# Kernel optimization log

Hardware: AMD Instinct MI355X
Metric: run time of the kernel (lower is better)

The kernel has to match this reference:

```python
import jax, jax.numpy as jnp
import numpy as np

T, IN, H, R = 8192, 256, 256, 4
MEM, MVD, OUT = 256, 128, 256


def lstm_scan(xs, Wih, Whh, b, reverse=False):
    # xs: [T, F]; torch LSTM gate order i, f, g, o; b = b_ih + b_hh combined
    Hh = Whh.shape[-1]

    def step(carry, x):
        h, c = carry
        z = Wih @ x + Whh @ h + b  # [4H]
        i, f, g, o = jnp.split(z, 4)
        c = jax.nn.sigmoid(f) * c + jax.nn.sigmoid(i) * jnp.tanh(g)
        h = jax.nn.sigmoid(o) * jnp.tanh(c)
        return (h, c), h

    init = (jnp.zeros((Hh,), xs.dtype), jnp.zeros((Hh,), xs.dtype))
    _, hs = jax.lax.scan(step, init, xs, reverse=reverse)
    return hs


def bilstm(xs, Wih, Whh, b):
    # Wih: [2, 4H, F] (dir 0 = forward, dir 1 = backward)
    hf = lstm_scan(xs, Wih[0], Whh[0], b[0])
    hb = lstm_scan(xs, Wih[1], Whh[1], b[1], reverse=True)
    return jnp.concatenate([hf, hb], axis=-1)


def setup_inputs() -> dict:
    key = jax.random.key(0)
    ks = jax.random.split(key, 24)
    s = 0.05
    d = {}
    d["inputs"] = jax.random.normal(ks[0], (T, IN), jnp.float32)
    d["edges"] = jax.random.randint(ks[1], (T, 2), 0, T)
    d["memory"] = jax.random.normal(ks[2], (T, MVD), jnp.float32)
    d["Wl_ih"] = jax.random.normal(ks[3], (2, 4 * H, IN)) * s
    d["Wl_hh"] = jax.random.normal(ks[4], (2, 4 * H, H)) * s
    d["bl"] = jax.random.normal(ks[5], (2, 4 * H)) * s
    d["Wh_ih"] = jax.random.normal(ks[6], (2, 4 * H, 2 * H)) * s
    d["Wh_hh"] = jax.random.normal(ks[7], (2, 4 * H, H)) * s
    d["bh"] = jax.random.normal(ks[8], (2, 4 * H)) * s
    d["Win"] = jax.random.normal(ks[9], (H, IN)) * s
    d["bin_"] = jax.random.normal(ks[10], (H,)) * s
    d["We"] = jax.random.normal(ks[11], (R, H, 2 * H)) * s
    d["be"] = jax.random.normal(ks[12], (R, H)) * s
    d["Wn_ih"] = jax.random.normal(ks[13], (R, 4 * H, IN + H)) * s
    d["Wn_hh"] = jax.random.normal(ks[14], (R, 4 * H, H)) * s
    d["bn"] = jax.random.normal(ks[15], (R, 4 * H)) * s
    d["Wmem"] = jax.random.normal(ks[16], (MEM, H)) * s
    d["bmem"] = jax.random.normal(ks[17], (MEM,)) * s
    d["Wc_ih"] = jax.random.normal(ks[18], (4 * H, IN + 2 * H + MVD)) * s
    d["Wc_hh"] = jax.random.normal(ks[19], (4 * H, H)) * s
    d["bc"] = jax.random.normal(ks[20], (4 * H,)) * s
    d["Wout"] = jax.random.normal(ks[21], (OUT, H)) * s
    d["bout"] = jax.random.normal(ks[22], (OUT,)) * s
    return d


def reference(inputs, edges, memory, Wl_ih, Wl_hh, bl, Wh_ih, Wh_hh, bh, Win, bin_, We, be, Wn_ih, Wn_hh, bn, Wmem, bmem, Wc_ih, Wc_hh, bc, Wout, bout):
    lower = bilstm(inputs, Wl_ih, Wl_hh, bl)          # [T, 2H]
    higher = bilstm(lower, Wh_ih, Wh_hh, bh)          # [T, 2H]
    nodes = inputs @ Win.T + bin_                     # [T, H]
    for r in range(We.shape[0]):                      # fixed small relation loop
        pair = jnp.concatenate([nodes[edges[:, 0]], nodes[edges[:, 1]]], axis=1)  # [T, 2H]
        eh = pair @ We[r].T + be[r]                   # [T, H]
        nodes = lstm_scan(jnp.concatenate([inputs, eh], axis=1), Wn_ih[r], Wn_hh[r], bn[r])
    memory_vector = nodes @ Wmem.T + bmem             # [T, MEM]
    ctrl_in = jnp.concatenate([inputs, higher, memory], axis=1)  # [T, IN+2H+MVD]
    out = lstm_scan(ctrl_in, Wc_ih, Wc_hh, bc)        # [T, H]
    out = out @ Wout.T + bout                         # [T, OUT]
    return out, memory_vector
```

## Files before the change

kernel.cpp:

```cpp
#include <hip/hip_runtime.h>
#include <cstdint>


#define T_LEN 8192
#define IN_F  256
#define HID   256
#define GATE  1024
#define NREL  4
#define OUT_N 256

typedef _Float16 half2_t __attribute__((ext_vector_type(2)));
typedef float    f32x4  __attribute__((ext_vector_type(4)));
typedef uint32_t u32x4  __attribute__((ext_vector_type(4)));
typedef short    s16x8  __attribute__((ext_vector_type(8)));

__device__ __forceinline__ float fdot2(uint32_t w, uint32_t h, float acc) {
#if __has_builtin(__builtin_amdgcn_fdot2)
  return __builtin_amdgcn_fdot2(__builtin_bit_cast(half2_t, w),
                                __builtin_bit_cast(half2_t, h), acc, false);
#else
  asm("v_dot2_f32_f16 %0, %1, %2, %0" : "+v"(acc) : "v"(w), "v"(h));
  return acc;
#endif
}

__device__ __forceinline__ float fsig(float x) { return 1.f / (1.f + __expf(-x)); }
__device__ __forceinline__ float ftanh(float x) { return 2.f / (1.f + __expf(-2.f * x)) - 1.f; }

__device__ __forceinline__ uint32_t pack2bf(float x, float y) {
  uint32_t ux = __builtin_bit_cast(uint32_t, x);
  uint32_t uy = __builtin_bit_cast(uint32_t, y);
  uint32_t rx = (ux + 0x7FFFu + ((ux >> 16) & 1u)) >> 16;
  uint32_t ry = (uy + 0x7FFFu + ((uy >> 16) & 1u)) >> 16;
  return (rx & 0xFFFFu) | (ry << 16);
}

__device__ __forceinline__ f32x4 mfma_bf(u32x4 a, u32x4 b, f32x4 c) {
  return __builtin_amdgcn_mfma_f32_16x16x32_bf16(
      __builtin_bit_cast(s16x8, a), __builtin_bit_cast(s16x8, b), c, 0, 0, 0);
}

__global__ void f2h_kernel(const float* __restrict__ in, _Float16* __restrict__ out, int n) {
  int i = blockIdx.x * blockDim.x + threadIdx.x;
  if (i < n) out[i] = (_Float16)in[i];
}

__global__ __launch_bounds__(256) void gemm16_kernel(
    const float* __restrict__ A, int lda,
    const float* __restrict__ W, int ldw,
    const float* __restrict__ bias, const float* addC,
    float* C, int ldc, int K) {
  __shared__ __align__(16) char As[4096];
  __shared__ __align__(16) char Bs[4096];
  const int tid = threadIdx.x;
  const int w = tid >> 6, l = tid & 63;
  const int m0 = blockIdx.y * 64, n0 = blockIdx.x * 64;

  const int srow = tid >> 2, skq = tid & 3;
  const int sbyte = (srow * 64 + skq * 16) ^ ((srow & 3) << 4);
  const float* Ap = A + (size_t)(m0 + srow) * lda + skq * 8;
  const float* Wp = W + (size_t)(n0 + srow) * ldw + skq * 8;

  const int fr = l & 15, kb = l >> 4;
  const int ar = w * 16 + fr;
  const int abyte  = (ar * 64 + kb * 16) ^ ((ar & 3) << 4);
  const int bbyte0 = ((fr)      * 64 + kb * 16) ^ ((fr & 3) << 4);
  const int bbyte1 = ((16 + fr) * 64 + kb * 16) ^ ((fr & 3) << 4);
  const int bbyte2 = ((32 + fr) * 64 + kb * 16) ^ ((fr & 3) << 4);
  const int bbyte3 = ((48 + fr) * 64 + kb * 16) ^ ((fr & 3) << 4);

  f32x4 acc0 = {0.f,0.f,0.f,0.f}, acc1 = {0.f,0.f,0.f,0.f};
  f32x4 acc2 = {0.f,0.f,0.f,0.f}, acc3 = {0.f,0.f,0.f,0.f};

  for (int k0 = 0; k0 < K; k0 += 32) {
    float4 a0 = *(const float4*)(Ap + k0);
    float4 a1 = *(const float4*)(Ap + k0 + 4);
    float4 w0 = *(const float4*)(Wp + k0);
    float4 w1 = *(const float4*)(Wp + k0 + 4);
    u32x4 pa = {pack2bf(a0.x,a0.y), pack2bf(a0.z,a0.w), pack2bf(a1.x,a1.y), pack2bf(a1.z,a1.w)};
    u32x4 pb = {pack2bf(w0.x,w0.y), pack2bf(w0.z,w0.w), pack2bf(w1.x,w1.y), pack2bf(w1.z,w1.w)};
    *(u32x4*)(As + sbyte) = pa;
    *(u32x4*)(Bs + sbyte) = pb;
    __syncthreads();
    u32x4 af  = *(const u32x4*)(As + abyte);
    u32x4 bf0 = *(const u32x4*)(Bs + bbyte0);
    u32x4 bf1 = *(const u32x4*)(Bs + bbyte1);
    u32x4 bf2 = *(const u32x4*)(Bs + bbyte2);
    u32x4 bf3 = *(const u32x4*)(Bs + bbyte3);
    acc0 = mfma_bf(af, bf0, acc0);
    acc1 = mfma_bf(af, bf1, acc1);
    acc2 = mfma_bf(af, bf2, acc2);
    acc3 = mfma_bf(af, bf3, acc3);
    __syncthreads();
  }

  const int col = l & 15;
  const int rb  = (l >> 4) * 4;
#define EPI(ct, ACC) { \
    int n = n0 + (ct) * 16 + col; \
    float bv = bias ? bias[n] : 0.f; \
    _Pragma("unroll") \
    for (int r = 0; r < 4; ++r) { \
      int m = m0 + w * 16 + rb + r; \
      float v = ACC[r] + bv; \
      if (addC) v += addC[(size_t)m * ldc + n]; \
      C[(size_t)m * ldc + n] = v; } }
  EPI(0, acc0) EPI(1, acc1) EPI(2, acc2) EPI(3, acc3)
#undef EPI
}

__global__ __launch_bounds__(256) void gemm_kernel(
    const float* __restrict__ A, int lda,
    const float* __restrict__ W, int ldw,
    const float* __restrict__ bias,
    const float* addC,
    float* C, int ldc, int M, int N, int K) {
  __shared__ float As[16][64];
  __shared__ float Bs[16][64];
  const int tid = threadIdx.x;
  const int tx = tid & 15, ty = tid >> 4;
  const int m0 = blockIdx.y * 64, n0 = blockIdx.x * 64;
  const int lr = tid >> 2;
  const int lc = (tid & 3) * 4;
  float acc[4][4] = {};
  for (int k0 = 0; k0 < K; k0 += 16) {
    float4 av = *(const float4*)&A[(size_t)(m0 + lr) * lda + k0 + lc];
    float4 wv = *(const float4*)&W[(size_t)(n0 + lr) * ldw + k0 + lc];
    As[lc + 0][lr] = av.x; As[lc + 1][lr] = av.y; As[lc + 2][lr] = av.z; As[lc + 3][lr] = av.w;
    Bs[lc + 0][lr] = wv.x; Bs[lc + 1][lr] = wv.y; Bs[lc + 2][lr] = wv.z; Bs[lc + 3][lr] = wv.w;
    __syncthreads();
#pragma unroll
    for (int k = 0; k < 16; ++k) {
      float a[4], b[4];
#pragma unroll
      for (int i = 0; i < 4; ++i) a[i] = As[k][ty * 4 + i];
#pragma unroll
      for (int jj = 0; jj < 4; ++jj) b[jj] = Bs[k][tx * 4 + jj];
#pragma unroll
      for (int i = 0; i < 4; ++i)
#pragma unroll
        for (int jj = 0; jj < 4; ++jj) acc[i][jj] += a[i] * b[jj];
    }
    __syncthreads();
  }
#pragma unroll
  for (int i = 0; i < 4; ++i) {
    int m = m0 + ty * 4 + i;
#pragma unroll
    for (int jj = 0; jj < 4; ++jj) {
      int n = n0 + tx * 4 + jj;
      float v = acc[i][jj];
      if (bias) v += bias[n];
      if (addC) v += addC[(size_t)m * ldc + n];
      C[(size_t)m * ldc + n] = v;
    }
  }
}

__global__ void gather_kernel(const float* __restrict__ nodes,
                              const int* __restrict__ edges,
                              float* __restrict__ pair) {
  int t = blockIdx.x;
  int c = threadIdx.x;
  int e = edges[t * 2 + (c >> 8)];
  pair[(size_t)t * 512 + c] = nodes[(size_t)e * 256 + (c & 255)];
}

struct ScanDesc {
  const float* Xp;
  const uint32_t* W;
  float* out;
  int rev;
  int hstride;
};

#define FOR24(M) M(0) M(1) M(2) M(3) M(4) M(5) M(6) M(7) M(8) M(9) M(10) M(11) \
                 M(12) M(13) M(14) M(15) M(16) M(17) M(18) M(19) M(20) M(21) M(22) M(23)

__global__
__attribute__((amdgpu_flat_work_group_size(512, 512), amdgpu_waves_per_eu(2)))
void lstm_scan2(ScanDesc d0, ScanDesc d1, ScanDesc d2, int T) {
  ScanDesc d;
  if (blockIdx.x == 0) d = d0;
  else if (blockIdx.x == 1) d = d1;
  else d = d2;
  const float* __restrict__ Xp = d.Xp;
  const uint32_t* __restrict__ W = d.W;
  float* __restrict__ out = d.out;
  const int rev = d.rev, hstride = d.hstride;

  const int j = threadIdx.x;
  __shared__ uint4 w_lds[2][8][512];
  __shared__ float z_lds[1024];
  __shared__ uint32_t h_lds[128];

  const uint4* wrow0 = (const uint4*)(W + (size_t)j * 128);
  const uint4* wrow1 = (const uint4*)(W + (size_t)(j + 512) * 128);

#define DECLW(i) uint4 wa##i, wb##i;
  FOR24(DECLW)
#undef DECLW
#define LOADW(i) wa##i = wrow0[i]; wb##i = wrow1[i];
  FOR24(LOADW)
#undef LOADW

#pragma unroll
  for (int q = 0; q < 8; ++q) w_lds[0][q][j] = wrow0[24 + q];
#pragma unroll
  for (int q = 0; q < 8; ++q) w_lds[1][q][j] = wrow1[24 + q];
  if (j < 128) h_lds[j] = 0u;
  float c = 0.f;
  __syncthreads();

  const int t0 = rev ? (T - 1) : 0;
  float xp0 = Xp[(size_t)t0 * GATE + j];
  float xp1 = Xp[(size_t)t0 * GATE + j + 512];

  for (int s = 0; s < T; ++s) {
    const int t = rev ? (T - 1 - s) : s;
    float a0 = xp0, a1 = 0.f, a2 = 0.f, a3 = 0.f;
    float b0 = xp1, b1 = 0.f, b2 = 0.f, b3 = 0.f;
    if (s + 1 < T) {
      const int tn = rev ? (t - 1) : (t + 1);
      xp0 = Xp[(size_t)tn * GATE + j];
      xp1 = Xp[(size_t)tn * GATE + j + 512];
    }

    const uint4* hq = (const uint4*)h_lds;
#define DOTQ(i) { uint4 hv = hq[i];                                   \
      a0 = fdot2(wa##i.x, hv.x, a0); b0 = fdot2(wb##i.x, hv.x, b0);   \
      a1 = fdot2(wa##i.y, hv.y, a1); b1 = fdot2(wb##i.y, hv.y, b1);   \
      a2 = fdot2(wa##i.z, hv.z, a2); b2 = fdot2(wb##i.z, hv.z, b2);   \
      a3 = fdot2(wa##i.w, hv.w, a3); b3 = fdot2(wb##i.w, hv.w, b3); }
    FOR24(DOTQ)
#undef DOTQ
#pragma unroll
    for (int q = 0; q < 8; ++q) {
      uint4 hv = hq[24 + q];
      uint4 wa = w_lds[0][q][j], wb = w_lds[1][q][j];
      a0 = fdot2(wa.x, hv.x, a0); b0 = fdot2(wb.x, hv.x, b0);
      a1 = fdot2(wa.y, hv.y, a1); b1 = fdot2(wb.y, hv.y, b1);
      a2 = fdot2(wa.z, hv.z, a2); b2 = fdot2(wb.z, hv.z, b2);
      a3 = fdot2(wa.w, hv.w, a3); b3 = fdot2(wb.w, hv.w, b3);
    }
    z_lds[j] = (a0 + a1) + (a2 + a3);
    z_lds[j + 512] = (b0 + b1) + (b2 + b3);
    __syncthreads();

    if (j < HID) {
      float zi = z_lds[j], zf = z_lds[j + 256], zg = z_lds[j + 512], zo = z_lds[j + 768];
      float ig = fsig(zi), fg = fsig(zf), gg = ftanh(zg), og = fsig(zo);
      c = fg * c + ig * gg;
      float h = og * ftanh(c);
      out[(size_t)t * hstride + j] = h;
      ((_Float16*)h_lds)[j] = (_Float16)h;
    }
    __syncthreads();
  }
}

extern "C" void kernel_launch(void* const* d_in, const int* in_sizes, int n_in,
                              void* d_out, int out_size, void* d_ws, size_t ws_size,
                              hipStream_t stream) {
  (void)in_sizes; (void)n_in; (void)out_size; (void)ws_size;
  const float* inputs = (const float*)d_in[0];
  const int*   edges  = (const int*)d_in[1];
  const float* memory = (const float*)d_in[2];
  const float* Wl_ih  = (const float*)d_in[3];
  const float* Wl_hh  = (const float*)d_in[4];
  const float* bl     = (const float*)d_in[5];
  const float* Wh_ih  = (const float*)d_in[6];
  const float* Wh_hh  = (const float*)d_in[7];
  const float* bh     = (const float*)d_in[8];
  const float* Win    = (const float*)d_in[9];
  const float* bin_   = (const float*)d_in[10];
  const float* We     = (const float*)d_in[11];
  const float* be     = (const float*)d_in[12];
  const float* Wn_ih  = (const float*)d_in[13];
  const float* Wn_hh  = (const float*)d_in[14];
  const float* bn     = (const float*)d_in[15];
  const float* Wmem   = (const float*)d_in[16];
  const float* bmem   = (const float*)d_in[17];
  const float* Wc_ih  = (const float*)d_in[18];
  const float* Wc_hh  = (const float*)d_in[19];
  const float* bc     = (const float*)d_in[20];
  const float* Wout   = (const float*)d_in[21];
  const float* bout   = (const float*)d_in[22];

  float* out_ptr = (float*)d_out;
  float* memvec  = out_ptr + (size_t)T_LEN * OUT_N;

  char* base = (char*)d_ws;
  size_t off = 0;
  auto carve = [&](size_t nbytes) -> void* {
    void* p = base + off; off += (nbytes + 255) & ~(size_t)255; return p;
  };
  float* XpA    = (float*)carve((size_t)T_LEN * GATE * 4);
  float* XpB    = (float*)carve((size_t)T_LEN * GATE * 4);
  float* XpC    = (float*)carve((size_t)T_LEN * GATE * 4);
  float* XpN    = (float*)carve((size_t)T_LEN * GATE * 4);
  float* lower  = (float*)carve((size_t)T_LEN * 512 * 4);
  float* higher = (float*)carve((size_t)T_LEN * 512 * 4);
  float* nodesA = (float*)carve((size_t)T_LEN * 256 * 4);
  float* nodesB = (float*)carve((size_t)T_LEN * 256 * 4);
  float* pairb  = (float*)carve((size_t)T_LEN * 512 * 4);
  float* ehb    = (float*)carve((size_t)T_LEN * 256 * 4);
  float* ctrlh  = (float*)carve((size_t)T_LEN * 256 * 4);
  uint32_t* Wl16 = (uint32_t*)carve((size_t)2 * GATE * HID * 2);
  uint32_t* Wh16 = (uint32_t*)carve((size_t)2 * GATE * HID * 2);
  uint32_t* Wn16 = (uint32_t*)carve((size_t)4 * GATE * HID * 2);
  uint32_t* Wc16 = (uint32_t*)carve((size_t)1 * GATE * HID * 2);
  const size_t WMAT = (size_t)GATE * HID / 2;

  auto f2h = [&](const float* src, uint32_t* dst, int n) {
    f2h_kernel<<<(n + 255) / 256, 256, 0, stream>>>(src, (_Float16*)dst, n);
  };
  f2h(Wl_hh, Wl16, 2 * GATE * HID);
  f2h(Wh_hh, Wh16, 2 * GATE * HID);
  f2h(Wn_hh, Wn16, 4 * GATE * HID);
  f2h(Wc_hh, Wc16, 1 * GATE * HID);

  auto gemm16 = [&](float* C, int ldc, const float* A, int lda,
                    const float* W, int ldw, const float* bias, const float* addC,
                    int M, int N, int K) {
    dim3 g(N / 64, M / 64);
    gemm16_kernel<<<g, 256, 0, stream>>>(A, lda, W, ldw, bias, addC, C, ldc, K);
  };
  auto gemm = [&](float* C, int ldc, const float* A, int lda,
                  const float* W, int ldw, const float* bias, const float* addC,
                  int M, int N, int K) {
    dim3 g(N / 64, M / 64);
    gemm_kernel<<<g, 256, 0, stream>>>(A, lda, W, ldw, bias, addC, C, ldc, M, N, K);
  };
  auto scan3 = [&](ScanDesc a, ScanDesc b, ScanDesc c, int nblk) {
    lstm_scan2<<<nblk, 512, 0, stream>>>(a, b, c, T_LEN);
  };
  ScanDesc dummy = {};

  gemm16(XpA, GATE, inputs, IN_F, Wl_ih,               IN_F, bl,        nullptr, T_LEN, GATE, IN_F);
  gemm16(XpB, GATE, inputs, IN_F, Wl_ih + GATE * IN_F, IN_F, bl + GATE, nullptr, T_LEN, GATE, IN_F);
  gemm16(nodesA, 256, inputs, IN_F, Win, IN_F, bin_, nullptr, T_LEN, 256, IN_F);
  gather_kernel<<<T_LEN, 512, 0, stream>>>(nodesA, edges, pairb);
  gemm16(ehb, 256, pairb, 512, We + (size_t)0 * HID * 512, 512, be + 0 * HID, nullptr, T_LEN, 256, 512);
  gemm16(XpN, GATE, inputs, IN_F, Wn_ih + (size_t)0 * GATE * 512,       512, bn + 0 * GATE, nullptr, T_LEN, GATE, IN_F);
  gemm16(XpN, GATE, ehb,    256,  Wn_ih + (size_t)0 * GATE * 512 + 256, 512, nullptr,       XpN,     T_LEN, GATE, 256);

  scan3({XpA, Wl16,        lower,       0, 512},
        {XpB, Wl16 + WMAT, lower + 256, 1, 512},
        {XpN, Wn16,        nodesB,      0, 256}, 3);

  gemm16(XpA, GATE, lower, 512, Wh_ih,              512, bh,        nullptr, T_LEN, GATE, 512);
  gemm16(XpB, GATE, lower, 512, Wh_ih + GATE * 512, 512, bh + GATE, nullptr, T_LEN, GATE, 512);
  gather_kernel<<<T_LEN, 512, 0, stream>>>(nodesB, edges, pairb);
  gemm16(ehb, 256, pairb, 512, We + (size_t)1 * HID * 512, 512, be + 1 * HID, nullptr, T_LEN, 256, 512);
  gemm16(XpN, GATE, inputs, IN_F, Wn_ih + (size_t)1 * GATE * 512,       512, bn + 1 * GATE, nullptr, T_LEN, GATE, IN_F);
  gemm16(XpN, GATE, ehb,    256,  Wn_ih + (size_t)1 * GATE * 512 + 256, 512, nullptr,       XpN,     T_LEN, GATE, 256);

  scan3({XpA, Wh16,        higher,       0, 512},
        {XpB, Wh16 + WMAT, higher + 256, 1, 512},
        {XpN, Wn16 + WMAT, nodesA,       0, 256}, 3);

  gemm16(XpC, GATE, inputs, IN_F, Wc_ih,       896, bc,      nullptr, T_LEN, GATE, IN_F);
  gemm16(XpC, GATE, memory, 128,  Wc_ih + 768, 896, nullptr, XpC,     T_LEN, GATE, 128);
  gemm16(XpC, GATE, higher, 512,  Wc_ih + 256, 896, nullptr, XpC,     T_LEN, GATE, 512);
  gather_kernel<<<T_LEN, 512, 0, stream>>>(nodesA, edges, pairb);
  gemm16(ehb, 256, pairb, 512, We + (size_t)2 * HID * 512, 512, be + 2 * HID, nullptr, T_LEN, 256, 512);
  gemm16(XpN, GATE, inputs, IN_F, Wn_ih + (size_t)2 * GATE * 512,       512, bn + 2 * GATE, nullptr, T_LEN, GATE, IN_F);
  gemm16(XpN, GATE, ehb,    256,  Wn_ih + (size_t)2 * GATE * 512 + 256, 512, nullptr,       XpN,     T_LEN, GATE, 256);

  scan3({XpN, Wn16 + 2 * WMAT, nodesB, 0, 256},
        {XpC, Wc16,            ctrlh,  0, 256}, dummy, 2);

  gather_kernel<<<T_LEN, 512, 0, stream>>>(nodesB, edges, pairb);
  gemm16(ehb, 256, pairb, 512, We + (size_t)3 * HID * 512, 512, be + 3 * HID, nullptr, T_LEN, 256, 512);
  gemm16(XpN, GATE, inputs, IN_F, Wn_ih + (size_t)3 * GATE * 512,       512, bn + 3 * GATE, nullptr, T_LEN, GATE, IN_F);
  gemm16(XpN, GATE, ehb,    256,  Wn_ih + (size_t)3 * GATE * 512 + 256, 512, nullptr,       XpN,     T_LEN, GATE, 256);

  scan3({XpN, Wn16 + 3 * WMAT, nodesA, 0, 256}, dummy, dummy, 1);

  gemm(memvec,  256, nodesA, 256, Wmem, HID, bmem, nullptr, T_LEN, 256, HID);
  gemm(out_ptr, 256, ctrlh,  256, Wout, HID, bout, nullptr, T_LEN, 256, HID);
}
```

Baseline: 64.01 ms.

## Split LSTM recurrent matvec across 4 lanes per row group with AGPR-pinned weights

```diff
diff --git a/kernel.cpp b/kernel.cpp
--- a/kernel.cpp
+++ b/kernel.cpp
@@ -174,12 +174,14 @@
   int hstride;
 };
 
-#define FOR24(M) M(0) M(1) M(2) M(3) M(4) M(5) M(6) M(7) M(8) M(9) M(10) M(11) \
-                 M(12) M(13) M(14) M(15) M(16) M(17) M(18) M(19) M(20) M(21) M(22) M(23)
+#define ARD(dst, src) asm volatile("v_accvgpr_read_b32 %0, %1" : "=v"(dst) : "a"(src))
+
+#define QPAIRS(M, ri) M(ri,0) M(ri,1) M(ri,2) M(ri,3) M(ri,4) M(ri,5) M(ri,6) M(ri,7)
+#define ALLRQ(M) QPAIRS(M,0) QPAIRS(M,1) QPAIRS(M,2) QPAIRS(M,3) QPAIRS(M,4) QPAIRS(M,5)
 
 __global__
 __attribute__((amdgpu_flat_work_group_size(512, 512), amdgpu_waves_per_eu(2)))
-void lstm_scan2(ScanDesc d0, ScanDesc d1, ScanDesc d2, int T) {
+void lstm_scan_ks(ScanDesc d0, ScanDesc d1, ScanDesc d2, int T) {
   ScanDesc d;
   if (blockIdx.x == 0) d = d0;
   else if (blockIdx.x == 1) d = d1;
@@ -189,74 +191,109 @@
   float* __restrict__ out = d.out;
   const int rev = d.rev, hstride = d.hstride;
 
-  const int j = threadIdx.x;
-  __shared__ uint4 w_lds[2][8][512];
+  const int tid = threadIdx.x;
+  const int s4 = tid & 3;
+  const int g  = tid >> 2;
+
+  __shared__ uint4 wl[16][512];
   __shared__ float z_lds[1024];
   __shared__ uint32_t h_lds[128];
 
-  const uint4* wrow0 = (const uint4*)(W + (size_t)j * 128);
-  const uint4* wrow1 = (const uint4*)(W + (size_t)(j + 512) * 128);
-
-#define DECLW(i) uint4 wa##i, wb##i;
-  FOR24(DECLW)
-#undef DECLW
-#define LOADW(i) wa##i = wrow0[i]; wb##i = wrow1[i];
-  FOR24(LOADW)
-#undef LOADW
-
-#pragma unroll
-  for (int q = 0; q < 8; ++q) w_lds[0][q][j] = wrow0[24 + q];
-#pragma unroll
-  for (int q = 0; q < 8; ++q) w_lds[1][q][j] = wrow1[24 + q];
-  if (j < 128) h_lds[j] = 0u;
+  const uint32_t* wr = W + (size_t)(g * 8) * 128 + s4 * 32;
+
+#define WDECL(ri, q) uint32_t w##ri##_##q##_0, w##ri##_##q##_1, w##ri##_##q##_2, w##ri##_##q##_3;
+  ALLRQ(WDECL)
+#undef WDECL
+#define WLOAD(ri, q) { uint4 t_ = ((const uint4*)(wr + (ri) * 128))[q]; \
+    w##ri##_##q##_0 = t_.x; w##ri##_##q##_1 = t_.y; \
+    w##ri##_##q##_2 = t_.z; w##ri##_##q##_3 = t_.w; }
+  ALLRQ(WLOAD)
+#undef WLOAD
+#define WPIN(ri, q) \
+    asm volatile("" : "+a"(w##ri##_##q##_0)); \
+    asm volatile("" : "+a"(w##ri##_##q##_1)); \
+    asm volatile("" : "+a"(w##ri##_##q##_2)); \
+    asm volatile("" : "+a"(w##ri##_##q##_3));
+  ALLRQ(WPIN)
+#undef WPIN
+
+  {
+    const uint4* wr6 = (const uint4*)(wr + 6 * 128);
+    const uint4* wr7 = (const uint4*)(wr + 7 * 128);
+#pragma unroll
+    for (int q = 0; q < 8; ++q) wl[q][tid] = wr6[q];
+#pragma unroll
+    for (int q = 0; q < 8; ++q) wl[8 + q][tid] = wr7[q];
+  }
+
+  if (tid < 128) h_lds[tid] = 0u;
   float c = 0.f;
+  const int t0 = rev ? (T - 1) : 0;
+  float xpi = 0.f, xpf = 0.f, xpg = 0.f, xpo = 0.f;
+  if (tid < HID) {
+    xpi = Xp[(size_t)t0 * GATE + tid];
+    xpf = Xp[(size_t)t0 * GATE + tid + 256];
+    xpg = Xp[(size_t)t0 * GATE + tid + 512];
+    xpo = Xp[(size_t)t0 * GATE + tid + 768];
+  }
   __syncthreads();
 
-  const int t0 = rev ? (T - 1) : 0;
-  float xp0 = Xp[(size_t)t0 * GATE + j];
-  float xp1 = Xp[(size_t)t0 * GATE + j + 512];
+  const uint4* hq = ((const uint4*)h_lds) + s4 * 8;
+
+#define DOTR(ri, q, hv) { uint32_t r0_, r1_, r2_, r3_; \
+    ARD(r0_, w##ri##_##q##_0); ARD(r1_, w##ri##_##q##_1); \
+    ARD(r2_, w##ri##_##q##_2); ARD(r3_, w##ri##_##q##_3); \
+    acc##ri = fdot2(r0_, hv.x, acc##ri); acc##ri = fdot2(r1_, hv.y, acc##ri); \
+    acc##ri = fdot2(r2_, hv.z, acc##ri); acc##ri = fdot2(r3_, hv.w, acc##ri); }
+#define QSTEP(q) { uint4 hv = hq[q]; \
+    DOTR(0, q, hv) DOTR(1, q, hv) DOTR(2, q, hv) \
+    DOTR(3, q, hv) DOTR(4, q, hv) DOTR(5, q, hv) \
+    { uint4 w6_ = wl[q][tid]; \
+      acc6 = fdot2(w6_.x, hv.x, acc6); acc6 = fdot2(w6_.y, hv.y, acc6); \
+      acc6 = fdot2(w6_.z, hv.z, acc6); acc6 = fdot2(w6_.w, hv.w, acc6); } \
+    { uint4 w7_ = wl[8 + q][tid]; \
+      acc7 = fdot2(w7_.x, hv.x, acc7); acc7 = fdot2(w7_.y, hv.y, acc7); \
+      acc7 = fdot2(w7_.z, hv.z, acc7); acc7 = fdot2(w7_.w, hv.w, acc7); } }
 
   for (int s = 0; s < T; ++s) {
     const int t = rev ? (T - 1 - s) : s;
-    float a0 = xp0, a1 = 0.f, a2 = 0.f, a3 = 0.f;
-    float b0 = xp1, b1 = 0.f, b2 = 0.f, b3 = 0.f;
-    if (s + 1 < T) {
-      const int tn = rev ? (t - 1) : (t + 1);
-      xp0 = Xp[(size_t)tn * GATE + j];
-      xp1 = Xp[(size_t)tn * GATE + j + 512];
-    }
-
-    const uint4* hq = (const uint4*)h_lds;
-#define DOTQ(i) { uint4 hv = hq[i];                                   \
-      a0 = fdot2(wa##i.x, hv.x, a0); b0 = fdot2(wb##i.x, hv.x, b0);   \
-      a1 = fdot2(wa##i.y, hv.y, a1); b1 = fdot2(wb##i.y, hv.y, b1);   \
-      a2 = fdot2(wa##i.z, hv.z, a2); b2 = fdot2(wb##i.z, hv.z, b2);   \
-      a3 = fdot2(wa##i.w, hv.w, a3); b3 = fdot2(wb##i.w, hv.w, b3); }
-    FOR24(DOTQ)
-#undef DOTQ
-#pragma unroll
-    for (int q = 0; q < 8; ++q) {
-      uint4 hv = hq[24 + q];
-      uint4 wa = w_lds[0][q][j], wb = w_lds[1][q][j];
-      a0 = fdot2(wa.x, hv.x, a0); b0 = fdot2(wb.x, hv.x, b0);
-      a1 = fdot2(wa.y, hv.y, a1); b1 = fdot2(wb.y, hv.y, b1);
-      a2 = fdot2(wa.z, hv.z, a2); b2 = fdot2(wb.z, hv.z, b2);
-      a3 = fdot2(wa.w, hv.w, a3); b3 = fdot2(wb.w, hv.w, b3);
-    }
-    z_lds[j] = (a0 + a1) + (a2 + a3);
-    z_lds[j + 512] = (b0 + b1) + (b2 + b3);
-    __syncthreads();
-
-    if (j < HID) {
-      float zi = z_lds[j], zf = z_lds[j + 256], zg = z_lds[j + 512], zo = z_lds[j + 768];
+    float acc0 = 0.f, acc1 = 0.f, acc2 = 0.f, acc3 = 0.f;
+    float acc4 = 0.f, acc5 = 0.f, acc6 = 0.f, acc7 = 0.f;
+
+    QSTEP(0) QSTEP(1) QSTEP(2) QSTEP(3)
+    QSTEP(4) QSTEP(5) QSTEP(6) QSTEP(7)
+
+#define RED(ri) acc##ri += __shfl_xor(acc##ri, 1, 64); \
+                acc##ri += __shfl_xor(acc##ri, 2, 64);
+    RED(0) RED(1) RED(2) RED(3) RED(4) RED(5) RED(6) RED(7)
+#undef RED
+
+    float za = (s4 == 0) ? acc0 : (s4 == 1) ? acc2 : (s4 == 2) ? acc4 : acc6;
+    float zb = (s4 == 0) ? acc1 : (s4 == 1) ? acc3 : (s4 == 2) ? acc5 : acc7;
+    *(float2*)&z_lds[(g << 3) + (s4 << 1)] = make_float2(za, zb);
+    __syncthreads();
+
+    if (tid < HID) {
+      float zi = z_lds[tid]       + xpi;
+      float zf = z_lds[tid + 256] + xpf;
+      float zg = z_lds[tid + 512] + xpg;
+      float zo = z_lds[tid + 768] + xpo;
       float ig = fsig(zi), fg = fsig(zf), gg = ftanh(zg), og = fsig(zo);
       c = fg * c + ig * gg;
       float h = og * ftanh(c);
-      out[(size_t)t * hstride + j] = h;
-      ((_Float16*)h_lds)[j] = (_Float16)h;
+      out[(size_t)t * hstride + tid] = h;
+      ((_Float16*)h_lds)[tid] = (_Float16)h;
+      int sn = (s + 1 < T) ? (s + 1) : s;
+      int tn = rev ? (T - 1 - sn) : sn;
+      xpi = Xp[(size_t)tn * GATE + tid];
+      xpf = Xp[(size_t)tn * GATE + tid + 256];
+      xpg = Xp[(size_t)tn * GATE + tid + 512];
+      xpo = Xp[(size_t)tn * GATE + tid + 768];
     }
     __syncthreads();
   }
+#undef QSTEP
+#undef DOTR
 }
 
 extern "C" void kernel_launch(void* const* d_in, const int* in_sizes, int n_in,
@@ -333,7 +370,7 @@
     gemm_kernel<<<g, 256, 0, stream>>>(A, lda, W, ldw, bias, addC, C, ldc, M, N, K);
   };
   auto scan3 = [&](ScanDesc a, ScanDesc b, ScanDesc c, int nblk) {
-    lstm_scan2<<<nblk, 512, 0, stream>>>(a, b, c, T_LEN);
+    lstm_scan_ks<<<nblk, 512, 0, stream>>>(a, b, c, T_LEN);
   };
   ScanDesc dummy = {};
 
```

Result: slower. 93.15 ms (+45.5%).
